# Optimization experiments

Measured on AMD Instinct MI355X. Metric: run time of the kernel, lower is better.

## Reference

```python
import jax, jax.numpy as jnp
import numpy as np

# Binarize: forward sign(x) in {-1,+1} (sign(0) -> +1), backward straight-through
# estimator (identity gradient), matching the standard ebnn Binarize autograd fn.
@jax.custom_vjp
def binarize(x):
    return jnp.where(x >= 0, 1.0, -1.0).astype(x.dtype)

def _bin_fwd(x):
    return binarize(x), None

def _bin_bwd(_, g):
    return (g,)  # straight-through

binarize.defvjp(_bin_fwd, _bin_bwd)


def setup_inputs() -> dict:
    key = jax.random.key(0)
    kx, kw = jax.random.split(key)
    N, Cin, H, W = 32, 256, 56, 56
    Cout, K = 256, 3
    x = jax.random.normal(kx, (N, Cin, H, W), dtype=jnp.float32)
    # xavier_normal init for conv weight
    fan_in = Cin * K * K
    fan_out = Cout * K * K
    std = float(np.sqrt(2.0 / (fan_in + fan_out)))
    w = jax.random.normal(kw, (Cout, Cin, K, K), dtype=jnp.float32) * std
    b = jnp.zeros((Cout,), dtype=jnp.float32)
    return {"x": x, "w": w, "b": b}


def reference(x, w, b):
    # binarize input (binarize_input=True) and weights, then standard conv2d
    xb = binarize(x)
    wb = binarize(w)
    out = jax.lax.conv_general_dilated(
        xb, wb,
        window_strides=(1, 1),
        padding=((1, 1), (1, 1)),
        rhs_dilation=(1, 1),
        dimension_numbers=("NCHW", "OIHW", "NCHW"),
        feature_group_count=1,
    )
    return out + b[None, :, None, None]
```

## Files before the change

kernel.cpp:

```cpp
#include <hip/hip_runtime.h>
#include <stdint.h>


#define NBATCH 32
#define CIN    256
#define COUT   256
#define HH     56
#define WW     56
#define HW     (HH*WW)
#define NPIX   (NBATCH*HW)

#define PW    58
#define PROW  (PW*8)
#define PIMG  (PW*PW*8)

#define XP_BYTES  ((size_t)NBATCH * PIMG * 4)
#define WQ_BYTES  ((size_t)9 * 8 * 256 * 32)

typedef int i32x4  __attribute__((ext_vector_type(4)));
typedef int i32x16 __attribute__((ext_vector_type(16)));

__global__ __launch_bounds__(256) void pack_x_kernel(
    const float* __restrict__ x, uint32_t* __restrict__ xp)
{
    int lane = threadIdx.x & 63;
    int wv   = threadIdx.x >> 6;
    int pix  = blockIdx.x * 64 + lane;
    int n  = pix / HW;
    int hw = pix - n * HW;
    int h  = hw / WW;
    int w_ = hw - h * WW;
    const float* xb = x + ((size_t)n * CIN + (size_t)wv * 64) * HW + hw;

    uint32_t w0 = 0, w1 = 0;
    #pragma unroll
    for (int j = 0; j < 32; ++j) {
        w0 |= (xb[(size_t)j * HW]        >= 0.0f ? 1u : 0u) << j;
        w1 |= (xb[(size_t)(j + 32) * HW] >= 0.0f ? 1u : 0u) << j;
    }
    uint32_t* dst = xp + (size_t)n * PIMG + (size_t)(h + 1) * PROW
                       + (size_t)(w_ + 1) * 8 + wv * 2;
    *(uint2*)dst = make_uint2(w0, w1);
}

__global__ __launch_bounds__(256) void pack_w2_kernel(
    const float* __restrict__ w, int8_t* __restrict__ wq)
{
    int co = blockIdx.x, ci = threadIdx.x;
    const float* wb = w + ((size_t)co * CIN + ci) * 9;
    int c8 = ci >> 5, s = ci & 31;
    #pragma unroll
    for (int t = 0; t < 9; ++t) {
        wq[((size_t)(t * 8 + c8) * 256 + co) * 32 + s] =
            (wb[t] >= 0.0f) ? (int8_t)1 : (int8_t)-1;
    }
}

__global__ __launch_bounds__(512, 4) void bconv_kernel(
    const uint32_t* __restrict__ xp, const int8_t* __restrict__ wq,
    const float* __restrict__ bias, float* __restrict__ out)
{
    __shared__ __align__(16) int8_t xt[4][66][256];
    __shared__ float bsh[256];

    int bx = blockIdx.x;
    int n  = bx / 28;
    int hb = bx - n * 28;
    int h  = hb * 2;
    int tid = threadIdx.x, lane = tid & 63, wv = tid >> 6;

    if (tid < 256) bsh[tid] = bias[tid];

    const uint32_t* xpb = xp + (size_t)n * PIMG;
    for (int e = tid; e < 4 * 66 * 64; e += 512) {
        int pr  = e / (66 * 64);
        int rem = e - pr * (66 * 64);
        int col = rem >> 6;
        int d   = rem & 63;
        int prg = h + pr;
        bool val = (prg >= 1) & (prg <= 56) & (col >= 1) & (col <= 56);
        uint32_t wvv = 0;
        if (val) wvv = xpb[(size_t)prg * PROW + col * 8 + (d >> 3)];
        uint32_t nib = (wvv >> ((d & 7) * 4)) & 0xFu;
        uint32_t sp  = (nib * 0x00204081u) & 0x01010101u;
        uint32_t o   = val ? __builtin_amdgcn_perm(0u, 0x000001FFu, sp) : 0u;
        uint32_t ba  = (uint32_t)((((pr * 66 + col) << 8) | (d << 2))
                                  ^ ((col & 7) << 4));
        *(uint32_t*)((char*)&xt[0][0][0] + ba) = o;
    }
    __syncthreads();

    i32x16 acc0 = {0}, acc1 = {0}, acc2 = {0}, acc3 = {0};

    int l31  = lane & 31;
    int hi16 = (lane >> 5) << 4;
    const int8_t* wql = wq + ((size_t)(wv * 32 + l31)) * 32 + hi16;
    const char* xtb = (const char*)&xt[0][0][0];

    for (int t = 0; t < 9; ++t) {
        int dh = (t * 11) >> 5;
        int dw = t - dh * 3;
        int c_ = l31 + dw;
        int sw = (c_ & 7) << 4;
        int ba0 = (dh * 66 + c_) << 8;
        int ba1 = ba0 + (32 << 8);
        int ba2 = ba0 + (66 << 8);
        int ba3 = ba2 + (32 << 8);
        const int8_t* wqt = wql + (size_t)t * 8 * 8192;
        #pragma unroll 4
        for (int c8 = 0; c8 < 8; ++c8) {
            i32x4 a = *(const i32x4*)(wqt + (size_t)c8 * 8192);
            int sx = ((c8 << 5) + hi16) ^ sw;
            i32x4 b0 = *(const i32x4*)(xtb + (sx + ba0));
            i32x4 b1 = *(const i32x4*)(xtb + (sx + ba1));
            i32x4 b2 = *(const i32x4*)(xtb + (sx + ba2));
            i32x4 b3 = *(const i32x4*)(xtb + (sx + ba3));
            acc0 = __builtin_amdgcn_mfma_i32_32x32x32_i8(a, b0, acc0, 0, 0, 0);
            acc1 = __builtin_amdgcn_mfma_i32_32x32x32_i8(a, b1, acc1, 0, 0, 0);
            acc2 = __builtin_amdgcn_mfma_i32_32x32x32_i8(a, b2, acc2, 0, 0, 0);
            acc3 = __builtin_amdgcn_mfma_i32_32x32x32_i8(a, b3, acc3, 0, 0, 0);
        }
    }

    #define EPI(ACC, PT) { \
        int pix = ((PT) & 1) * 32 + l31; \
        if (pix < WW) { \
            int hg = h + ((PT) >> 1); \
            float* op = out + (size_t)n * COUT * HW + (size_t)hg * WW + pix; \
            _Pragma("unroll") \
            for (int r = 0; r < 16; ++r) { \
                int row = (r & 3) + 8 * (r >> 2) + ((lane >> 5) << 2); \
                int co  = (wv << 5) + row; \
                op[(size_t)co * HW] = (float)ACC[r] + bsh[co]; \
            } \
        } }
    EPI(acc0, 0) EPI(acc1, 1) EPI(acc2, 2) EPI(acc3, 3)
    #undef EPI
}

extern "C" void kernel_launch(void* const* d_in, const int* in_sizes, int n_in,
                              void* d_out, int out_size, void* d_ws, size_t ws_size,
                              hipStream_t stream) {
    const float* x = (const float*)d_in[0];
    const float* w = (const float*)d_in[1];
    const float* b = (const float*)d_in[2];
    float* out = (float*)d_out;

    uint32_t* xp = (uint32_t*)d_ws;
    int8_t*   wq = (int8_t*)((char*)d_ws + XP_BYTES);

    pack_x_kernel<<<NPIX / 64, 256, 0, stream>>>(x, xp);
    pack_w2_kernel<<<COUT, 256, 0, stream>>>(w, wq);

    bconv_kernel<<<NBATCH * (HH / 2), 512, 0, stream>>>(xp, wq, b, out);
}
```

Before: 108.6 us.

## Reuse shared-memory input fragments across kernel rows and widen LDS swizzle

The tap loop is restructured so that, for each column offset dw, the input fragments for the four padded rows are loaded once and shared across the three kernel-row taps (dh). This cuts LDS reads per MFMA from one per MFMA to about two-thirds of one. The XOR swizzle grows from 8 to 16 columns to reduce bank conflicts, which matters because lanes now span 32 consecutive columns. In exchange, more live B registers and three weight loads per iteration raise register pressure under the launch bound of 4 blocks.

```diff
diff --git a/kernel.cpp b/kernel.cpp
--- a/kernel.cpp
+++ b/kernel.cpp
@@ -85,7 +85,7 @@
         uint32_t sp  = (nib * 0x00204081u) & 0x01010101u;
         uint32_t o   = val ? __builtin_amdgcn_perm(0u, 0x000001FFu, sp) : 0u;
         uint32_t ba  = (uint32_t)((((pr * 66 + col) << 8) | (d << 2))
-                                  ^ ((col & 7) << 4));
+                                  ^ ((col & 15) << 4));
         *(uint32_t*)((char*)&xt[0][0][0] + ba) = o;
     }
     __syncthreads();
@@ -97,28 +97,38 @@
     const int8_t* wql = wq + ((size_t)(wv * 32 + l31)) * 32 + hi16;
     const char* xtb = (const char*)&xt[0][0][0];
 
-    for (int t = 0; t < 9; ++t) {
-        int dh = (t * 11) >> 5;
-        int dw = t - dh * 3;
-        int c_ = l31 + dw;
-        int sw = (c_ & 7) << 4;
-        int ba0 = (dh * 66 + c_) << 8;
-        int ba1 = ba0 + (32 << 8);
-        int ba2 = ba0 + (66 << 8);
-        int ba3 = ba2 + (32 << 8);
-        const int8_t* wqt = wql + (size_t)t * 8 * 8192;
-        #pragma unroll 4
+    for (int dw = 0; dw < 3; ++dw) {
+        int c0 = l31 + dw;
+        int sw = (c0 & 15) << 4;
+        const char* xc = xtb + (c0 << 8);
+        const int8_t* wa0 = wql + (size_t)(dw * 8) * 8192;
+        #pragma unroll
         for (int c8 = 0; c8 < 8; ++c8) {
-            i32x4 a = *(const i32x4*)(wqt + (size_t)c8 * 8192);
             int sx = ((c8 << 5) + hi16) ^ sw;
-            i32x4 b0 = *(const i32x4*)(xtb + (sx + ba0));
-            i32x4 b1 = *(const i32x4*)(xtb + (sx + ba1));
-            i32x4 b2 = *(const i32x4*)(xtb + (sx + ba2));
-            i32x4 b3 = *(const i32x4*)(xtb + (sx + ba3));
-            acc0 = __builtin_amdgcn_mfma_i32_32x32x32_i8(a, b0, acc0, 0, 0, 0);
-            acc1 = __builtin_amdgcn_mfma_i32_32x32x32_i8(a, b1, acc1, 0, 0, 0);
-            acc2 = __builtin_amdgcn_mfma_i32_32x32x32_i8(a, b2, acc2, 0, 0, 0);
-            acc3 = __builtin_amdgcn_mfma_i32_32x32x32_i8(a, b3, acc3, 0, 0, 0);
+            i32x4 b00 = *(const i32x4*)(xc + ((0 * 66     ) << 8) + sx);
+            i32x4 b01 = *(const i32x4*)(xc + ((0 * 66 + 32) << 8) + sx);
+            i32x4 b10 = *(const i32x4*)(xc + ((1 * 66     ) << 8) + sx);
+            i32x4 b11 = *(const i32x4*)(xc + ((1 * 66 + 32) << 8) + sx);
+            i32x4 b20 = *(const i32x4*)(xc + ((2 * 66     ) << 8) + sx);
+            i32x4 b21 = *(const i32x4*)(xc + ((2 * 66 + 32) << 8) + sx);
+            i32x4 b30 = *(const i32x4*)(xc + ((3 * 66     ) << 8) + sx);
+            i32x4 b31 = *(const i32x4*)(xc + ((3 * 66 + 32) << 8) + sx);
+            const int8_t* wa = wa0 + (size_t)c8 * 8192;
+            i32x4 a0v = *(const i32x4*)(wa);
+            i32x4 a1v = *(const i32x4*)(wa + 196608);
+            i32x4 a2v = *(const i32x4*)(wa + 393216);
+            acc0 = __builtin_amdgcn_mfma_i32_32x32x32_i8(a0v, b00, acc0, 0, 0, 0);
+            acc1 = __builtin_amdgcn_mfma_i32_32x32x32_i8(a0v, b01, acc1, 0, 0, 0);
+            acc2 = __builtin_amdgcn_mfma_i32_32x32x32_i8(a0v, b10, acc2, 0, 0, 0);
+            acc3 = __builtin_amdgcn_mfma_i32_32x32x32_i8(a0v, b11, acc3, 0, 0, 0);
+            acc0 = __builtin_amdgcn_mfma_i32_32x32x32_i8(a1v, b10, acc0, 0, 0, 0);
+            acc1 = __builtin_amdgcn_mfma_i32_32x32x32_i8(a1v, b11, acc1, 0, 0, 0);
+            acc2 = __builtin_amdgcn_mfma_i32_32x32x32_i8(a1v, b20, acc2, 0, 0, 0);
+            acc3 = __builtin_amdgcn_mfma_i32_32x32x32_i8(a1v, b21, acc3, 0, 0, 0);
+            acc0 = __builtin_amdgcn_mfma_i32_32x32x32_i8(a2v, b20, acc0, 0, 0, 0);
+            acc1 = __builtin_amdgcn_mfma_i32_32x32x32_i8(a2v, b21, acc1, 0, 0, 0);
+            acc2 = __builtin_amdgcn_mfma_i32_32x32x32_i8(a2v, b30, acc2, 0, 0, 0);
+            acc3 = __builtin_amdgcn_mfma_i32_32x32x32_i8(a2v, b31, acc3, 0, 0, 0);
         }
     }
 
```

Result: faster. 105.7 us (-2.7%).

## Restructure conv tile so each wave reuses shared-memory fragments across rows and channels

Applied to the files above, without the earlier changes.

Drops the block to 4 waves, each computing 64 output channels by 64 pixels by 2 rows with eight accumulators. Each shared-memory B fragment is now loaded once per input row and reused across the vertical taps and both channel groups, which cuts LDS reads per MFMA. The LDS swizzle is widened from 8 to 16 columns to reduce bank conflicts. The cost is higher register pressure and half the threads doing the shared-memory fill.

```diff
diff --git a/kernel.cpp b/kernel.cpp
--- a/kernel.cpp
+++ b/kernel.cpp
@@ -56,7 +56,10 @@
     }
 }
 
-__global__ __launch_bounds__(512, 4) void bconv_kernel(
+#define MFMA(ACC, A, B) \
+    ACC = __builtin_amdgcn_mfma_i32_32x32x32_i8(A, B, ACC, 0, 0, 0);
+
+__global__ __launch_bounds__(256, 2) void bconv_kernel(
     const uint32_t* __restrict__ xp, const int8_t* __restrict__ wq,
     const float* __restrict__ bias, float* __restrict__ out)
 {
@@ -69,10 +72,10 @@
     int h  = hb * 2;
     int tid = threadIdx.x, lane = tid & 63, wv = tid >> 6;
 
-    if (tid < 256) bsh[tid] = bias[tid];
+    bsh[tid] = bias[tid];
 
     const uint32_t* xpb = xp + (size_t)n * PIMG;
-    for (int e = tid; e < 4 * 66 * 64; e += 512) {
+    for (int e = tid; e < 4 * 66 * 64; e += 256) {
         int pr  = e / (66 * 64);
         int rem = e - pr * (66 * 64);
         int col = rem >> 6;
@@ -85,57 +88,79 @@
         uint32_t sp  = (nib * 0x00204081u) & 0x01010101u;
         uint32_t o   = val ? __builtin_amdgcn_perm(0u, 0x000001FFu, sp) : 0u;
         uint32_t ba  = (uint32_t)((((pr * 66 + col) << 8) | (d << 2))
-                                  ^ ((col & 7) << 4));
+                                  ^ ((col & 15) << 4));
         *(uint32_t*)((char*)&xt[0][0][0] + ba) = o;
     }
     __syncthreads();
 
-    i32x16 acc0 = {0}, acc1 = {0}, acc2 = {0}, acc3 = {0};
-
     int l31  = lane & 31;
     int hi16 = (lane >> 5) << 4;
-    const int8_t* wql = wq + ((size_t)(wv * 32 + l31)) * 32 + hi16;
-    const char* xtb = (const char*)&xt[0][0][0];
+    const char* wql0 = (const char*)wq + (size_t)(wv * 64 + l31) * 32 + hi16;
+    const char* wql1 = wql0 + 1024;
+    const char* xtb  = (const char*)&xt[0][0][0];
 
-    for (int t = 0; t < 9; ++t) {
-        int dh = (t * 11) >> 5;
-        int dw = t - dh * 3;
-        int c_ = l31 + dw;
-        int sw = (c_ & 7) << 4;
-        int ba0 = (dh * 66 + c_) << 8;
-        int ba1 = ba0 + (32 << 8);
-        int ba2 = ba0 + (66 << 8);
-        int ba3 = ba2 + (32 << 8);
-        const int8_t* wqt = wql + (size_t)t * 8 * 8192;
-        #pragma unroll 4
+    i32x16 p00 = {0}, p01 = {0}, p10 = {0}, p11 = {0};
+    i32x16 q00 = {0}, q01 = {0}, q10 = {0}, q11 = {0};
+
+    #pragma unroll 1
+    for (int dw = 0; dw < 3; ++dw) {
+        int col0 = l31 + dw;
+        int sw   = (col0 & 15) << 4;
+        const char* xc0 = xtb + (col0 << 8);
+        const char* xc1 = xc0 + (32 << 8);
+        #pragma unroll
         for (int c8 = 0; c8 < 8; ++c8) {
-            i32x4 a = *(const i32x4*)(wqt + (size_t)c8 * 8192);
             int sx = ((c8 << 5) + hi16) ^ sw;
-            i32x4 b0 = *(const i32x4*)(xtb + (sx + ba0));
-            i32x4 b1 = *(const i32x4*)(xtb + (sx + ba1));
-            i32x4 b2 = *(const i32x4*)(xtb + (sx + ba2));
-            i32x4 b3 = *(const i32x4*)(xtb + (sx + ba3));
-            acc0 = __builtin_amdgcn_mfma_i32_32x32x32_i8(a, b0, acc0, 0, 0, 0);
-            acc1 = __builtin_amdgcn_mfma_i32_32x32x32_i8(a, b1, acc1, 0, 0, 0);
-            acc2 = __builtin_amdgcn_mfma_i32_32x32x32_i8(a, b2, acc2, 0, 0, 0);
-            acc3 = __builtin_amdgcn_mfma_i32_32x32x32_i8(a, b3, acc3, 0, 0, 0);
+            i32x4 b00 = *(const i32x4*)(xc0 + ((0 * 66) << 8) + sx);
+            i32x4 b01 = *(const i32x4*)(xc0 + ((1 * 66) << 8) + sx);
+            i32x4 b02 = *(const i32x4*)(xc0 + ((2 * 66) << 8) + sx);
+            i32x4 b03 = *(const i32x4*)(xc0 + ((3 * 66) << 8) + sx);
+            i32x4 b10 = *(const i32x4*)(xc1 + ((0 * 66) << 8) + sx);
+            i32x4 b11 = *(const i32x4*)(xc1 + ((1 * 66) << 8) + sx);
+            i32x4 b12 = *(const i32x4*)(xc1 + ((2 * 66) << 8) + sx);
+            i32x4 b13 = *(const i32x4*)(xc1 + ((3 * 66) << 8) + sx);
+            const char* wa0 = wql0 + (size_t)(dw * 8 + c8) * 8192;
+            const char* wa1 = wql1 + (size_t)(dw * 8 + c8) * 8192;
+            i32x4 a00 = *(const i32x4*)(wa0);
+            i32x4 a01 = *(const i32x4*)(wa0 + 196608);
+            i32x4 a02 = *(const i32x4*)(wa0 + 393216);
+            i32x4 a10 = *(const i32x4*)(wa1);
+            i32x4 a11 = *(const i32x4*)(wa1 + 196608);
+            i32x4 a12 = *(const i32x4*)(wa1 + 393216);
+
+            MFMA(p00, a00, b00) MFMA(p01, a00, b01)
+            MFMA(p10, a10, b00) MFMA(p11, a10, b01)
+            MFMA(p00, a01, b01) MFMA(p01, a01, b02)
+            MFMA(p10, a11, b01) MFMA(p11, a11, b02)
+            MFMA(p00, a02, b02) MFMA(p01, a02, b03)
+            MFMA(p10, a12, b02) MFMA(p11, a12, b03)
+            MFMA(q00, a00, b10) MFMA(q01, a00, b11)
+            MFMA(q10, a10, b10) MFMA(q11, a10, b11)
+            MFMA(q00, a01, b11) MFMA(q01, a01, b12)
+            MFMA(q10, a11, b11) MFMA(q11, a11, b12)
+            MFMA(q00, a02, b12) MFMA(q01, a02, b13)
+            MFMA(q10, a12, b12) MFMA(q11, a12, b13)
         }
     }
 
-    #define EPI(ACC, PT) { \
-        int pix = ((PT) & 1) * 32 + l31; \
+    #define EPI2(P0, P1, CG, PIXB) { \
+        int pix = (PIXB) + l31; \
         if (pix < WW) { \
-            int hg = h + ((PT) >> 1); \
-            float* op = out + (size_t)n * COUT * HW + (size_t)hg * WW + pix; \
+            float* op = out + (size_t)n * COUT * HW + (size_t)h * WW + pix; \
             _Pragma("unroll") \
             for (int r = 0; r < 16; ++r) { \
                 int row = (r & 3) + 8 * (r >> 2) + ((lane >> 5) << 2); \
-                int co  = (wv << 5) + row; \
-                op[(size_t)co * HW] = (float)ACC[r] + bsh[co]; \
+                int co  = ((2 * wv + (CG)) << 5) + row; \
+                float bb = bsh[co]; \
+                op[(size_t)co * HW]      = (float)P0[r] + bb; \
+                op[(size_t)co * HW + WW] = (float)P1[r] + bb; \
             } \
         } }
-    EPI(acc0, 0) EPI(acc1, 1) EPI(acc2, 2) EPI(acc3, 3)
-    #undef EPI
+    EPI2(p00, p01, 0, 0)
+    EPI2(p10, p11, 1, 0)
+    EPI2(q00, q01, 0, 32)
+    EPI2(q10, q11, 1, 32)
+    #undef EPI2
 }
 
 extern "C" void kernel_launch(void* const* d_in, const int* in_sizes, int n_in,
@@ -152,5 +177,5 @@
     pack_x_kernel<<<NPIX / 64, 256, 0, stream>>>(x, xp);
     pack_w2_kernel<<<COUT, 256, 0, stream>>>(w, wq);
 
-    bconv_kernel<<<NBATCH * (HH / 2), 512, 0, stream>>>(xp, wq, b, out);
+    bconv_kernel<<<NBATCH * (HH / 2), 256, 0, stream>>>(xp, wq, b, out);
 }
```

Result: slower. 128.2 us (+18.1%).
